# Optimization experiments

Hardware: AMD Instinct MI355X
Metric: run time of the kernel (lower is better)

## Reference

```python
import jax, jax.numpy as jnp
import numpy as np
from jax import lax

VOCAB, EMBED_DIM, NUM_TAGS = 50000, 300, 16
BATCH, SEQ = 64, 512


def setup_inputs() -> dict:
    key = jax.random.key(0)
    k0, k1, k2, k3, k4 = jax.random.split(key, 5)
    text = jax.random.randint(k0, (BATCH, SEQ), 0, VOCAB)
    tags = jax.random.randint(k1, (BATCH, SEQ), 0, NUM_TAGS)
    embed_table = jax.random.normal(k2, (VOCAB, EMBED_DIM), jnp.float32) * 0.02
    W = jax.random.normal(k3, (EMBED_DIM, NUM_TAGS), jnp.float32) * 0.05
    b = jnp.zeros((NUM_TAGS,), jnp.float32)
    trans = jax.random.uniform(k4, (NUM_TAGS, NUM_TAGS), jnp.float32)
    return {"text": text, "tags": tags, "embed_table": embed_table, "W": W, "b": b, "trans": trans}


def crf_log_likelihood(probs, tags, lens, trans):
    # probs: [B,S,T] unary potentials; tags: [B,S] int; lens: [B]; trans: [T,T]
    B, S, T = probs.shape
    t_idx = jnp.arange(S)
    mask = (t_idx[None, :] < lens[:, None])  # [B,S] valid positions

    # --- gold sequence score ---
    unary = jnp.take_along_axis(probs, tags[..., None], axis=2)[..., 0]  # [B,S]
    unary_score = jnp.sum(unary * mask, axis=1)
    btrans = trans[tags[:, :-1], tags[:, 1:]]            # [B,S-1]
    bmask = mask[:, 1:]                                   # transition t->t+1 valid iff t+1 < len
    binary_score = jnp.sum(btrans * bmask, axis=1)

    # --- forward algorithm (log partition) ---
    alpha0 = probs[:, 0]                                  # [B,T]
    emits = jnp.moveaxis(probs[:, 1:], 0, 1)              # [S-1,B,T]
    ms = jnp.moveaxis(mask[:, 1:], 0, 1)                  # [S-1,B]

    def step(alpha, inp):
        emit, m = inp
        new = jax.nn.logsumexp(alpha[:, :, None] + trans[None, :, :], axis=1) + emit
        return jnp.where(m[:, None], new, alpha), None

    alpha, _ = lax.scan(step, alpha0, (emits, ms))
    log_norm = jax.nn.logsumexp(alpha, axis=-1)           # [B]
    return unary_score + binary_score - log_norm


def reference(text, tags, embed_table, W, b, trans):
    # dropout is identity in eval/reference mode
    text_lens = jnp.sum((text != 0).astype(jnp.int32), axis=1)  # [B]
    probs = embed_table[text] @ W + b                            # [B,S,T]
    log_likelihood = crf_log_likelihood(probs, tags, text_lens, trans)
    return probs, text_lens, log_likelihood
```

## Files before the change

### kernel.cpp

```cpp
#include <hip/hip_runtime.h>
#include <hip/hip_bf16.h>

#define VOCAB 50000
#define ED    300
#define NT    16
#define BB    64
#define SS    512

#define LOG2E 1.4426950408889634f
#define LN2   0.6931471805599453f

__global__ __launch_bounds__(256) void probs_kernel(const int* __restrict__ text,
                                                    const float* __restrict__ emb,
                                                    const float* __restrict__ W,
                                                    const float* __restrict__ bias,
                                                    float* __restrict__ out_probs) {
  const int tid = threadIdx.x;
  const int lane = tid & 63, wave = tid >> 6;
  const int r = lane >> 4, t = lane & 15;
  const int row = blockIdx.x * 16 + wave * 4 + r;

  const int tok = text[row];
  const float4* erow = (const float4*)(emb + (size_t)tok * ED);

  float acc = bias[t];
#pragma unroll 5
  for (int c = 0; c < 75; ++c) {
    float4 e = erow[c];
    const float* wp = W + (size_t)(4 * c) * NT + t;
    acc = fmaf(e.x, wp[0],      acc);
    acc = fmaf(e.y, wp[NT],     acc);
    acc = fmaf(e.z, wp[2 * NT], acc);
    acc = fmaf(e.w, wp[3 * NT], acc);
  }
  out_probs[(size_t)row * NT + t] = acc;
}

template <int CTRL>
__device__ __forceinline__ float dppmov(float x) {
  int xi = __float_as_int(x);
  return __int_as_float(
      __builtin_amdgcn_update_dpp(xi, xi, CTRL, 0xF, 0xF, false));
}

__device__ __forceinline__ float crf_step(float g, float pe, const float E[16]) {
  float gn, h, m, c, a1, a2, a3;
  asm("s_nop 1\n\t"
      "v_mov_b32_dpp %[h], %[g] row_half_mirror row_mask:0xf bank_mask:0xf\n\t"
      "v_mov_b32_dpp %[m], %[g] row_mirror row_mask:0xf bank_mask:0xf\n\t"
      "v_mul_f32 %[gn], %[g], %[e0]\n\t"
      "v_fmac_f32_dpp %[gn], %[g], %[e1] quad_perm:[1,0,3,2] row_mask:0xf bank_mask:0xf\n\t"
      "v_fmac_f32_dpp %[gn], %[g], %[e2] quad_perm:[2,3,0,1] row_mask:0xf bank_mask:0xf\n\t"
      "v_fmac_f32_dpp %[gn], %[g], %[e3] quad_perm:[3,2,1,0] row_mask:0xf bank_mask:0xf\n\t"
      "v_mov_b32_dpp %[c], %[m] row_half_mirror row_mask:0xf bank_mask:0xf\n\t"
      "v_mul_f32 %[a1], %[h], %[e7]\n\t"
      "v_fmac_f32_dpp %[a1], %[h], %[e6] quad_perm:[1,0,3,2] row_mask:0xf bank_mask:0xf\n\t"
      "v_fmac_f32_dpp %[a1], %[h], %[e5] quad_perm:[2,3,0,1] row_mask:0xf bank_mask:0xf\n\t"
      "v_fmac_f32_dpp %[a1], %[h], %[e4] quad_perm:[3,2,1,0] row_mask:0xf bank_mask:0xf\n\t"
      "v_mul_f32 %[a2], %[m], %[e15]\n\t"
      "v_fmac_f32_dpp %[a2], %[m], %[e14] quad_perm:[1,0,3,2] row_mask:0xf bank_mask:0xf\n\t"
      "v_fmac_f32_dpp %[a2], %[m], %[e13] quad_perm:[2,3,0,1] row_mask:0xf bank_mask:0xf\n\t"
      "v_fmac_f32_dpp %[a2], %[m], %[e12] quad_perm:[3,2,1,0] row_mask:0xf bank_mask:0xf\n\t"
      "v_mul_f32 %[a3], %[c], %[e8]\n\t"
      "v_fmac_f32_dpp %[a3], %[c], %[e9] quad_perm:[1,0,3,2] row_mask:0xf bank_mask:0xf\n\t"
      "v_fmac_f32_dpp %[a3], %[c], %[e10] quad_perm:[2,3,0,1] row_mask:0xf bank_mask:0xf\n\t"
      "v_fmac_f32_dpp %[a3], %[c], %[e11] quad_perm:[3,2,1,0] row_mask:0xf bank_mask:0xf\n\t"
      "v_add_f32 %[gn], %[gn], %[a1]\n\t"
      "v_add_f32 %[a2], %[a2], %[a3]\n\t"
      "v_add_f32 %[gn], %[gn], %[a2]\n\t"
      "v_mul_f32 %[gn], %[gn], %[pe]"
      : [gn] "=&v"(gn), [h] "=&v"(h), [m] "=&v"(m), [c] "=&v"(c),
        [a1] "=&v"(a1), [a2] "=&v"(a2), [a3] "=&v"(a3)
      : [g] "v"(g), [pe] "v"(pe),
        [e0] "v"(E[0]), [e1] "v"(E[1]), [e2] "v"(E[2]), [e3] "v"(E[3]),
        [e4] "v"(E[4]), [e5] "v"(E[5]), [e6] "v"(E[6]), [e7] "v"(E[7]),
        [e8] "v"(E[8]), [e9] "v"(E[9]), [e10] "v"(E[10]), [e11] "v"(E[11]),
        [e12] "v"(E[12]), [e13] "v"(E[13]), [e14] "v"(E[14]), [e15] "v"(E[15]));
  return gn;
}

__global__ __launch_bounds__(64) void crf_kernel(const int* __restrict__ text,
                                                 const int* __restrict__ tags,
                                                 const float* __restrict__ trans,
                                                 const float* __restrict__ probs,
                                                 float* __restrict__ out_lens,
                                                 float* __restrict__ out_ll) {
  __shared__ float lps[SS * NT];
  __shared__ int tgs[SS];
  __shared__ float trs[256];

  const int tid = threadIdx.x;
  const int j = tid & 15;
  const int b = blockIdx.x;

  {
    const float4* p4 = (const float4*)(probs + (size_t)b * SS * NT);
    float4* l4 = (float4*)lps;
#pragma unroll
    for (int i = 0; i < 32; ++i) {
      float4 v = p4[tid + 64 * i];
      v.x *= LOG2E; v.y *= LOG2E; v.z *= LOG2E; v.w *= LOG2E;
      l4[tid + 64 * i] = v;
    }
    const int4* t4 = (const int4*)(tags + b * SS);
    int4* lt = (int4*)tgs;
#pragma unroll
    for (int i = 0; i < 2; ++i) lt[tid + 64 * i] = t4[tid + 64 * i];
    for (int i = tid; i < 256; i += 64) trs[i] = trans[i];
  }
  __syncthreads();

  const int* tx = text + b * SS;
  int cnt = 0;
#pragma unroll
  for (int k = 0; k < 8; ++k) cnt += (tx[tid + 64 * k] != 0) ? 1 : 0;
  for (int off = 32; off > 0; off >>= 1) cnt += __shfl_xor(cnt, off, 64);
  const int len = cnt;
  if (tid == 0) out_lens[b] = (float)len;

  float su = 0.f, sb = 0.f;
#pragma unroll
  for (int it = 0; it < 8; ++it) {
    const int s = tid + 64 * it;
    if (s < len) {
      int t1 = tgs[s];
      su += lps[s * NT + t1];
      if (s >= 1) sb += trs[tgs[s - 1] * 16 + t1];
    }
  }
  float sc = fmaf(su, LN2, sb);
  for (int off = 32; off > 0; off >>= 1) sc += __shfl_xor(sc, off, 64);

  float E[16];
#pragma unroll
  for (int k = 0; k < 16; ++k) E[k] = __expf(trs[((j ^ k) << 4) + j]);

  float g = exp2f(lps[j]);
  float K2 = 0.f;

  float raw[16];
#pragma unroll
  for (int c = 0; c < 16; ++c) raw[c] = lps[(1 + c) * NT + j];

  for (int blk = 0; blk < 31; ++blk) {
#pragma unroll
    for (int c = 0; c < 16; ++c) {
      const int s = 1 + blk * 16 + c;
      float pe = exp2f(raw[c]);
      int spre = s + 16; if (spre > 511) spre = 511;
      raw[c] = lps[spre * NT + j];
      float gn = crf_step(g, pe, E);
      g = (s < len) ? gn : g;
    }
    float mx = g;
    mx = fmaxf(mx, dppmov<0xB1>(mx));
    mx = fmaxf(mx, dppmov<0x4E>(mx));
    mx = fmaxf(mx, dppmov<0x141>(mx));
    mx = fmaxf(mx, dppmov<0x140>(mx));
    float rr = 1.0f / mx;
    K2 -= __log2f(rr);
    g *= rr;
  }
#pragma unroll
  for (int c = 0; c < 15; ++c) {
    const int s = 497 + c;
    float pe = exp2f(raw[c]);
    float gn = crf_step(g, pe, E);
    g = (s < len) ? gn : g;
  }

  float x = g;
  x += dppmov<0xB1>(x);
  x += dppmov<0x4E>(x);
  x += dppmov<0x141>(x);
  x += dppmov<0x140>(x);
  float log_norm = LN2 * (K2 + __log2f(x));
  if (tid == 0) out_ll[b] = sc - log_norm;
}

extern "C" void kernel_launch(void* const* d_in, const int* in_sizes, int n_in,
                              void* d_out, int out_size, void* d_ws, size_t ws_size,
                              hipStream_t stream) {
  const int* text = (const int*)d_in[0];
  const int* tags = (const int*)d_in[1];
  const float* emb = (const float*)d_in[2];
  const float* W = (const float*)d_in[3];
  const float* bias = (const float*)d_in[4];
  const float* trans = (const float*)d_in[5];

  float* out = (float*)d_out;
  float* out_probs = out;
  float* out_lens = out + BB * SS * NT;
  float* out_ll = out + BB * SS * NT + BB;

  probs_kernel<<<(BB * SS) / 16, 256, 0, stream>>>(text, emb, W, bias, out_probs);
  crf_kernel<<<BB, 64, 0, stream>>>(text, tags, trans, out_probs, out_lens, out_ll);
}
```

Before: 169.8 us.

## Stage transposed W in LDS for probs and trim CRF scan to sequence length

```diff
diff --git a/kernel.cpp b/kernel.cpp
--- a/kernel.cpp
+++ b/kernel.cpp
@@ -10,28 +10,45 @@
 #define LOG2E 1.4426950408889634f
 #define LN2   0.6931471805599453f
 
+#define WSTR 308
+
 __global__ __launch_bounds__(256) void probs_kernel(const int* __restrict__ text,
                                                     const float* __restrict__ emb,
                                                     const float* __restrict__ W,
                                                     const float* __restrict__ bias,
                                                     float* __restrict__ out_probs) {
+  __shared__ float wt[NT * WSTR];
+
   const int tid = threadIdx.x;
   const int lane = tid & 63, wave = tid >> 6;
   const int r = lane >> 4, t = lane & 15;
   const int row = blockIdx.x * 16 + wave * 4 + r;
 
+  for (int e = tid; e < ED * NT; e += 256) {
+    int d = e >> 4, tt = e & 15;
+    wt[tt * WSTR + d] = W[e];
+  }
+
   const int tok = text[row];
   const float4* erow = (const float4*)(emb + (size_t)tok * ED);
-
   float acc = bias[t];
-#pragma unroll 5
+
+  float4 A[8];
+#pragma unroll
+  for (int i = 0; i < 8; ++i) A[i] = erow[i];
+
+  __syncthreads();
+
+  const float4* w4 = (const float4*)(wt + t * WSTR);
+#pragma unroll
   for (int c = 0; c < 75; ++c) {
-    float4 e = erow[c];
-    const float* wp = W + (size_t)(4 * c) * NT + t;
-    acc = fmaf(e.x, wp[0],      acc);
-    acc = fmaf(e.y, wp[NT],     acc);
-    acc = fmaf(e.z, wp[2 * NT], acc);
-    acc = fmaf(e.w, wp[3 * NT], acc);
+    float4 e = A[c % 8];
+    if (c < 67) A[c % 8] = erow[c + 8];
+    float4 w = w4[c];
+    acc = fmaf(e.x, w.x, acc);
+    acc = fmaf(e.y, w.y, acc);
+    acc = fmaf(e.z, w.z, acc);
+    acc = fmaf(e.w, w.w, acc);
   }
   out_probs[(size_t)row * NT + t] = acc;
 }
@@ -85,7 +102,7 @@
                                                  const float* __restrict__ probs,
                                                  float* __restrict__ out_lens,
                                                  float* __restrict__ out_ll) {
-  __shared__ float lps[SS * NT];
+  __shared__ float lps[(SS + 1) * NT];
   __shared__ int tgs[SS];
   __shared__ float trs[256];
 
@@ -138,19 +155,21 @@
   float g = exp2f(lps[j]);
   float K2 = 0.f;
 
+  const int T = (len > 0) ? len - 1 : 0;
+  const int nfull = T >> 4;
+  const int rem = T & 15;
+
   float raw[16];
 #pragma unroll
   for (int c = 0; c < 16; ++c) raw[c] = lps[(1 + c) * NT + j];
 
-  for (int blk = 0; blk < 31; ++blk) {
+  int s0 = 1;
+  for (int blk = 0; blk < nfull; ++blk) {
 #pragma unroll
     for (int c = 0; c < 16; ++c) {
-      const int s = 1 + blk * 16 + c;
       float pe = exp2f(raw[c]);
-      int spre = s + 16; if (spre > 511) spre = 511;
-      raw[c] = lps[spre * NT + j];
-      float gn = crf_step(g, pe, E);
-      g = (s < len) ? gn : g;
+      raw[c] = lps[(s0 + 16 + c) * NT + j];
+      g = crf_step(g, pe, E);
     }
     float mx = g;
     mx = fmaxf(mx, dppmov<0xB1>(mx));
@@ -160,13 +179,11 @@
     float rr = 1.0f / mx;
     K2 -= __log2f(rr);
     g *= rr;
-  }
-#pragma unroll
-  for (int c = 0; c < 15; ++c) {
-    const int s = 497 + c;
+    s0 += 16;
+  }
+  for (int c = 0; c < rem; ++c) {
     float pe = exp2f(raw[c]);
-    float gn = crf_step(g, pe, E);
-    g = (s < len) ? gn : g;
+    g = crf_step(g, pe, E);
   }
 
   float x = g;
```

Measured after the change: 151.7 us. -10.7%, faster.
